# Kernel optimization log

Measured on AMD Instinct MI355X. Metric: run time of the kernel, lower is better.

Reference implementation:

```python
import jax, jax.numpy as jnp
import numpy as np

THRESHOLD = 0.1


def setup_inputs() -> dict:
    key = jax.random.key(0)
    kq, kr, ki = jax.random.split(key, 3)
    H, Q, K, I, D = 4, 64, 64, 2048, 128  # heads, queries, index_dim, items, d_model
    query = jax.random.normal(kq, (H, Q, K), dtype=jnp.float32)
    record = jax.random.normal(kr, (I, D), dtype=jnp.float32)
    index = jax.random.normal(ki, (I, K), dtype=jnp.float32)
    return {"query": query, "record": record, "index": index}


def reference(query, record, index):
    # query: (H, Q, K); record: (I, D); index: (I, K)
    H = query.shape[-3]
    # fp16 score matmul, cast back to fp32 (matches torch .type(float16) / .type(float32))
    q16 = query.astype(jnp.float16)
    i16 = index.astype(jnp.float16)
    score = jnp.matmul(q16, jnp.swapaxes(i16, -1, -2)).astype(jnp.float32)  # (H, Q, I)
    score = jnp.swapaxes(score, -3, -2)                      # (Q, H, I)
    score = score.reshape(score.shape[:-2] + (-1,))          # (Q, H*I), flat idx = h*I + i

    passed = score > THRESHOLD                               # (Q, H*I)

    # record tiled over heads so that flat index h*I + i -> record[i]
    records = jnp.tile(record, (H, 1))                       # (H*I, D)

    # activated records: relu(score)-scaled record, zeroed where below threshold
    act = jnp.where(passed[..., None],
                    jax.nn.relu(score)[..., None] * records,
                    jnp.zeros((), dtype=record.dtype))       # (Q, H*I, D)

    # stable sort bringing passing items to the front (torch: argsort(passed, descending));
    # we keep full width (max_item = H*I) so shapes are static under jit; the tail
    # beyond the data-dependent max_passed of the torch code is exactly zero anyway.
    order = jnp.argsort(jnp.where(passed, 0, 1).astype(jnp.int32),
                        axis=-1, stable=True)                # (Q, H*I)
    passing_records = jnp.take_along_axis(act, order[..., None], axis=-2)  # (Q, H*I, D)

    return passing_records, score
```

## Files before the change

kernel.cpp:

```cpp
#include <hip/hip_runtime.h>
#include <hip/hip_fp16.h>

#define NH 4
#define NQ 64
#define NK 64
#define NI 2048
#define ND 128
#define NHI (NH * NI)
#define REC_ELEMS ((size_t)NQ * NHI * ND)

typedef float f32x4 __attribute__((ext_vector_type(4)));

__global__ __launch_bounds__(64) void score_kernel(
    const float* __restrict__ query,
    const float* __restrict__ index,
    float* __restrict__ score_out) {
#pragma clang fp contract(off)
  const int b     = blockIdx.x;
  const int h     = b >> 6;
  const int ic    = b & 63;
  const int lane  = threadIdx.x;
  const int qbase = (lane >> 5) * 32;
  const int i     = ic * 32 + (lane & 31);

  __shared__ float qs[NQ * NK];
  const float* qg = query + (size_t)h * NQ * NK;
  for (int j = 0; j < 64; ++j) {
    const int idx = j * 64 + lane;
    qs[idx] = __half2float(__float2half(qg[idx]));
  }
  __syncthreads();

  float r[NK];
  const float4* row4 = (const float4*)(index + (size_t)i * NK);
#pragma unroll
  for (int c = 0; c < 16; ++c) {
    float4 v = row4[c];
    r[c * 4 + 0] = __half2float(__float2half(v.x));
    r[c * 4 + 1] = __half2float(__float2half(v.y));
    r[c * 4 + 2] = __half2float(__float2half(v.z));
    r[c * 4 + 3] = __half2float(__float2half(v.w));
  }

#pragma unroll 4
  for (int qi = 0; qi < 32; ++qi) {
    const int q = qbase + qi;
    const float* qrow = qs + q * NK;
    float acc = 0.0f;
#pragma unroll
    for (int k = 0; k < NK; ++k)
      acc = acc + qrow[k] * r[k];
    score_out[(size_t)q * NHI + h * NI + i] = __half2float(__float2half(acc));
  }
}

__global__ __launch_bounds__(256) void compact_kernel(
    const float* __restrict__ score,
    int* __restrict__ comp,
    int* __restrict__ npass) {
  const int q = blockIdx.x;
  const int t = threadIdx.x;
  const float* srow = score + (size_t)q * NHI;
  const int base = t * 32;

  float s[32];
  const float4* s4 = (const float4*)(srow + base);
#pragma unroll
  for (int j4 = 0; j4 < 8; ++j4) {
    float4 v = s4[j4];
    s[j4 * 4 + 0] = v.x; s[j4 * 4 + 1] = v.y;
    s[j4 * 4 + 2] = v.z; s[j4 * 4 + 3] = v.w;
  }

  int cnt = 0;
#pragma unroll
  for (int j = 0; j < 32; ++j) cnt += (s[j] > 0.1f) ? 1 : 0;

  __shared__ int cs[256];
  cs[t] = cnt;
  __syncthreads();
  for (int off = 1; off < 256; off <<= 1) {
    int v = (t >= off) ? cs[t - off] : 0;
    __syncthreads();
    cs[t] += v;
    __syncthreads();
  }
  int pos = cs[t] - cnt;
  int* crow = comp + (size_t)q * NHI;
#pragma unroll
  for (int j = 0; j < 32; ++j) {
    if (s[j] > 0.1f) crow[pos++] = base + j;
  }
  if (t == 255) npass[q] = cs[255];
}

__global__ __launch_bounds__(256) void write_kernel(
    const float* __restrict__ score,
    const float* __restrict__ record,
    const int* __restrict__ comp,
    const int* __restrict__ npass,
    float* __restrict__ out) {
  const int lane = threadIdx.x & 63;
  const int half = lane >> 5;
  const int l32  = lane & 31;
  const int wave = blockIdx.x * 4 + (threadIdx.x >> 6);
  const size_t r0 = (size_t)wave << 6;
  const int q  = (int)(r0 >> 13);
  const int p0 = (int)(r0 & (NHI - 1));

  int pass_rows = npass[q] - p0;
  pass_rows = pass_rows < 0 ? 0 : (pass_rows > 64 ? 64 : pass_rows);

  int   j_lane = 0;
  float s_lane = 0.0f;
  if (lane < pass_rows) {
    j_lane = comp[r0 + lane];
    s_lane = score[((size_t)q << 13) + j_lane];
  }

  float* outbase = out + (r0 << 7);
#pragma unroll 4
  for (int i = 0; i < 32; ++i) {
    const int ro = 2 * i + half;
    const int   j = __shfl(j_lane, ro);
    const float s = __shfl(s_lane, ro);
    f32x4 val = {0.0f, 0.0f, 0.0f, 0.0f};
    if (ro < pass_rows) {
      const f32x4* rec = (const f32x4*)(record + ((size_t)(j & (NI - 1)) << 7));
      val = s * rec[l32];
    }
    *((f32x4*)(outbase + ((size_t)ro << 7)) + l32) = val;
  }
}

extern "C" void kernel_launch(void* const* d_in, const int* in_sizes, int n_in,
                              void* d_out, int out_size, void* d_ws, size_t ws_size,
                              hipStream_t stream) {
  const float* query  = (const float*)d_in[0];
  const float* record = (const float*)d_in[1];
  const float* index  = (const float*)d_in[2];

  float* out       = (float*)d_out;
  float* score_out = out + REC_ELEMS;

  int* comp  = (int*)d_ws;
  int* npass = comp + (size_t)NQ * NHI;

  score_kernel<<<NH * 64, 64, 0, stream>>>(query, index, score_out);
  compact_kernel<<<NQ, 256, 0, stream>>>(score_out, comp, npass);
  write_kernel<<<2048, 256, 0, stream>>>(score_out, record, comp, npass, out);
}
```

Measured before the change: 71.21 us.

## Widen score and compact blocks; split write loop into gather and zero-fill phases

The score kernel now uses 256 threads per block, each computing 8 queries instead of 32, and loads the query tile into shared memory with float4 accesses. The compact kernel uses 512 threads with 16 elements each, so the per-row scan is spread over more threads. The write kernel splits its loop into a gather phase over the passing rows, an odd-row tail, and a pure zero-store phase, removing the per-row branch and the record loads for the zero region. More threads add scan steps and barrier cost in the compact kernel, and the variable trip counts can hurt unrolling.

```diff
diff --git a/kernel.cpp b/kernel.cpp
--- a/kernel.cpp
+++ b/kernel.cpp
@@ -11,23 +11,29 @@
 
 typedef float f32x4 __attribute__((ext_vector_type(4)));
 
-__global__ __launch_bounds__(64) void score_kernel(
+__global__ __launch_bounds__(256) void score_kernel(
     const float* __restrict__ query,
     const float* __restrict__ index,
     float* __restrict__ score_out) {
 #pragma clang fp contract(off)
-  const int b     = blockIdx.x;
-  const int h     = b >> 6;
-  const int ic    = b & 63;
-  const int lane  = threadIdx.x;
-  const int qbase = (lane >> 5) * 32;
-  const int i     = ic * 32 + (lane & 31);
+  const int b      = blockIdx.x;
+  const int h      = b >> 6;
+  const int ic     = b & 63;
+  const int t      = threadIdx.x;
+  const int i      = ic * 32 + (t & 31);
+  const int qbase  = (t >> 5) * 8;
 
   __shared__ float qs[NQ * NK];
-  const float* qg = query + (size_t)h * NQ * NK;
-  for (int j = 0; j < 64; ++j) {
-    const int idx = j * 64 + lane;
-    qs[idx] = __half2float(__float2half(qg[idx]));
+  {
+    const float4* qg4 = (const float4*)(query + (size_t)h * NQ * NK);
+    float4* qs4 = (float4*)qs;
+#pragma unroll
+    for (int c = 0; c < 4; ++c) {
+      float4 v = qg4[c * 256 + t];
+      qs4[c * 256 + t] = make_float4(
+          __half2float(__float2half(v.x)), __half2float(__float2half(v.y)),
+          __half2float(__float2half(v.z)), __half2float(__float2half(v.w)));
+    }
   }
   __syncthreads();
 
@@ -42,8 +48,8 @@
     r[c * 4 + 3] = __half2float(__float2half(v.w));
   }
 
-#pragma unroll 4
-  for (int qi = 0; qi < 32; ++qi) {
+#pragma unroll
+  for (int qi = 0; qi < 8; ++qi) {
     const int q = qbase + qi;
     const float* qrow = qs + q * NK;
     float acc = 0.0f;
@@ -54,19 +60,19 @@
   }
 }
 
-__global__ __launch_bounds__(256) void compact_kernel(
+__global__ __launch_bounds__(512) void compact_kernel(
     const float* __restrict__ score,
     int* __restrict__ comp,
     int* __restrict__ npass) {
   const int q = blockIdx.x;
   const int t = threadIdx.x;
+  const int base = t * 16;
   const float* srow = score + (size_t)q * NHI;
-  const int base = t * 32;
 
-  float s[32];
+  float s[16];
   const float4* s4 = (const float4*)(srow + base);
 #pragma unroll
-  for (int j4 = 0; j4 < 8; ++j4) {
+  for (int j4 = 0; j4 < 4; ++j4) {
     float4 v = s4[j4];
     s[j4 * 4 + 0] = v.x; s[j4 * 4 + 1] = v.y;
     s[j4 * 4 + 2] = v.z; s[j4 * 4 + 3] = v.w;
@@ -74,12 +80,12 @@
 
   int cnt = 0;
 #pragma unroll
-  for (int j = 0; j < 32; ++j) cnt += (s[j] > 0.1f) ? 1 : 0;
+  for (int j = 0; j < 16; ++j) cnt += (s[j] > 0.1f) ? 1 : 0;
 
-  __shared__ int cs[256];
+  __shared__ int cs[512];
   cs[t] = cnt;
   __syncthreads();
-  for (int off = 1; off < 256; off <<= 1) {
+  for (int off = 1; off < 512; off <<= 1) {
     int v = (t >= off) ? cs[t - off] : 0;
     __syncthreads();
     cs[t] += v;
@@ -88,10 +94,10 @@
   int pos = cs[t] - cnt;
   int* crow = comp + (size_t)q * NHI;
 #pragma unroll
-  for (int j = 0; j < 32; ++j) {
+  for (int j = 0; j < 16; ++j) {
     if (s[j] > 0.1f) crow[pos++] = base + j;
   }
-  if (t == 255) npass[q] = cs[255];
+  if (t == 511) npass[q] = cs[511];
 }
 
 __global__ __launch_bounds__(256) void write_kernel(
@@ -119,17 +125,36 @@
   }
 
   float* outbase = out + (r0 << 7);
+  const int fp = pass_rows >> 1;
+
 #pragma unroll 4
-  for (int i = 0; i < 32; ++i) {
+  for (int i = 0; i < fp; ++i) {
     const int ro = 2 * i + half;
     const int   j = __shfl(j_lane, ro);
     const float s = __shfl(s_lane, ro);
+    const f32x4* rec = (const f32x4*)(record + ((size_t)(j & (NI - 1)) << 7));
+    f32x4 val = s * rec[l32];
+    *((f32x4*)(outbase + ((size_t)ro << 7)) + l32) = val;
+  }
+
+  if (pass_rows & 1) {
+    const int ro = 2 * fp + half;
+    const int   j = __shfl(j_lane, ro);
+    const float s = __shfl(s_lane, ro);
     f32x4 val = {0.0f, 0.0f, 0.0f, 0.0f};
-    if (ro < pass_rows) {
+    if (half == 0) {
       const f32x4* rec = (const f32x4*)(record + ((size_t)(j & (NI - 1)) << 7));
       val = s * rec[l32];
     }
     *((f32x4*)(outbase + ((size_t)ro << 7)) + l32) = val;
+  }
+
+  const int zstart = fp + (pass_rows & 1);
+  const f32x4 z = {0.0f, 0.0f, 0.0f, 0.0f};
+#pragma unroll 8
+  for (int i = zstart; i < 32; ++i) {
+    const int ro = 2 * i + half;
+    *((f32x4*)(outbase + ((size_t)ro << 7)) + l32) = z;
   }
 }
 
@@ -146,7 +171,7 @@
   int* comp  = (int*)d_ws;
   int* npass = comp + (size_t)NQ * NHI;
 
-  score_kernel<<<NH * 64, 64, 0, stream>>>(query, index, score_out);
-  compact_kernel<<<NQ, 256, 0, stream>>>(score_out, comp, npass);
+  score_kernel<<<NH * 64, 256, 0, stream>>>(query, index, score_out);
+  compact_kernel<<<NQ, 512, 0, stream>>>(score_out, comp, npass);
   write_kernel<<<2048, 256, 0, stream>>>(score_out, record, comp, npass, out);
 }
```

New measurement: 64.20 us. 9.8% less time.
